# Optimization experiments

Hardware: AMD Instinct MI355X
Metric: run time of the kernel (lower is better)

The kernel has to match this reference:

```python
import jax, jax.numpy as jnp
import numpy as np
from jax import lax

B, F_BINS, T = 4, 128, 16384
J_T, N_W, KF, KT = 4, 8, 33, 129


def setup_inputs() -> dict:
    key = jax.random.key(0)
    k1, k2, k3 = jax.random.split(key, 3)
    x = jax.random.normal(k1, (B, F_BINS, T), dtype=jnp.float32)
    # complex Morlet-style wavelet bank parameters: [J_t, n_w, kf, kt]
    wav_real = jax.random.normal(k2, (J_T, N_W, KF, KT), dtype=jnp.float32) * 0.05
    wav_imag = jax.random.normal(k3, (J_T, N_W, KF, KT), dtype=jnp.float32) * 0.05
    return {"x": x, "wav_real": wav_real, "wav_imag": wav_imag}


def _avg_pool_last(x, w):
    # non-overlapping mean pooling along the last (time) axis, stride == window
    if w == 1:
        return x
    shp = x.shape
    return x.reshape(shp[:-1] + (shp[-1] // w, w)).mean(axis=-1)


def reference(x, wav_real, wav_imag):
    # x: [B, F, T]; wav_real/wav_imag: [J_t, n_w, kf, kt]
    J_t, n_w = wav_real.shape[0], wav_real.shape[1]
    # avg_win_t cascade: 2**J_t halving each octave -> [16, 8, 4, 2]
    avg_wins_t = [2 ** (J_t - j) for j in range(J_t)]
    xi = x[:, None]  # [B, 1, F, T_cur]
    octaves = []
    for j in range(J_t):
        # stack real and imag kernels as 2*n_w output channels of one conv2d
        k = jnp.concatenate([wav_real[j], wav_imag[j]], axis=0)[:, None]  # [2*n_w, 1, kf, kt]
        o = lax.conv_general_dilated(
            xi, k, window_strides=(1, 1), padding='SAME',
            dimension_numbers=('NCHW', 'OIHW', 'NCHW'))  # [B, 2*n_w, F, T_cur]
        # complex modulus (x is real, kernel complex): |conv_r + i*conv_i|
        mod = jnp.sqrt(o[:, :n_w] ** 2 + o[:, n_w:] ** 2)  # [B, n_w, F, T_cur]
        w = avg_wins_t[j]
        octaves.append(_avg_pool_last(mod, w))  # [B, n_w, F, T//2**J_t]
        if w > 1:
            xi = _avg_pool_last(xi, 2)  # decimate input in time by 2
    # all octaves share the same pooled time length -> concat on channel dim
    return jnp.concatenate(octaves, axis=1)  # [B, J_t*n_w, F, T//2**J_t]
```

## Files before the change

kernel.cpp:

```cpp
#include <hip/hip_runtime.h>
#include <math.h>

#define B_      4
#define F_BINS  128
#define T_FULL  16384
#define NW      8
#define KF      33
#define KT      129

#define TT      128
#define ROWS    260
#define PITCH   72
#define DTP     136
#define D2      48

typedef __attribute__((ext_vector_type(8))) short short8;
typedef __attribute__((ext_vector_type(4))) float f32x4;
typedef uint uint4a16 __attribute__((ext_vector_type(4), aligned(16)));

union ABFrag { uint4a16 u; short8 v; };

__device__ __forceinline__ ushort f2bf(float v) {
  unsigned u = __float_as_uint(v);
  unsigned r = (u + 0x7FFFu + ((u >> 16) & 1u)) >> 16;
  return (ushort)r;
}

__device__ __forceinline__ short8 load_a16(const ushort* p) {
  ABFrag f; f.u = *(const uint4a16*)p; return f.v;
}

__device__ __forceinline__ short8 mkG(short8 a, short8 b) {
  return __builtin_shufflevector(a, b, 4, 5, 6, 7, 8, 9, 10, 11);
}

__global__ __launch_bounds__(256) void prep_w(
    const float* __restrict__ wr, const float* __restrict__ wi,
    ushort* __restrict__ wq) {
  int idx = blockIdx.x * 256 + threadIdx.x;
  int d2  = idx % D2;
  int dt  = (idx / D2) % DTP;
  int ch  = (idx / (D2 * DTP)) % 16;
  int gam = (idx / (D2 * DTP * 16)) % 4;
  int oct = idx / (D2 * DTP * 16 * 4);
  int df  = d2 - 4 - gam;
  float v = 0.f;
  if (df >= 0 && df < KF && dt < KT) {
    const float* src = (ch < 8) ? wr : wi;
    v = src[(((size_t)oct * 8 + (ch & 7)) * KF + df) * KT + dt];
  }
  wq[idx] = f2bf(v);
}

__global__ __launch_bounds__(256) void prep_x(
    const float* __restrict__ x,
    ushort* __restrict__ xT0, ushort* __restrict__ xT1,
    ushort* __restrict__ xT2, ushort* __restrict__ xT3) {
  __shared__ float lt[128 * 65];
  const int b  = blockIdx.y;
  const int t0 = blockIdx.x * 64;
  const int tid = threadIdx.x;
  const int wv = tid >> 6, lane = tid & 63;
#pragma unroll
  for (int rep = 0; rep < 32; ++rep) {
    int f = rep * 4 + wv;
    lt[f * 65 + lane] = x[((size_t)b * 128 + f) * T_FULL + t0 + lane];
  }
  __syncthreads();
  ushort* dst[4] = {xT0, xT1, xT2, xT3};
  const int Ts[4] = {16384, 8192, 4096, 2048};
  for (int lvl = 0; lvl < 4; ++lvl) {
    int nt = 64 >> lvl, w = 1 << lvl;
    float inv = 1.f / (float)w;
    int tasks = nt * 16;
    for (int i = tid; i < tasks; i += 256) {
      int tl = i >> 4, fc = i & 15;
      __align__(16) ushort vs[8];
#pragma unroll
      for (int e = 0; e < 8; ++e) {
        float a = 0.f;
        for (int m = 0; m < w; ++m) a += lt[(fc * 8 + e) * 65 + tl * w + m];
        vs[e] = f2bf(a * inv);
      }
      ushort* pdst = dst[lvl] + ((size_t)b * Ts[lvl] + (t0 >> lvl) + tl) * 128 + fc * 8;
      *(uint4*)pdst = *(const uint4*)vs;
    }
  }
}

__global__ __launch_bounds__(256, 3) void conv_mfma(
    const ushort* __restrict__ xT0, const ushort* __restrict__ xT1,
    const ushort* __restrict__ xT2, const ushort* __restrict__ xT3,
    const ushort* __restrict__ wq, float* __restrict__ out) {
  __shared__ ushort xt[ROWS * PITCH];
  const int tid = threadIdx.x;
  const int bx = blockIdx.x;

  int oct, local;
  if (bx < 2048)      { oct = 0; local = bx; }
  else if (bx < 3072) { oct = 1; local = bx - 2048; }
  else if (bx < 3584) { oct = 2; local = bx - 3072; }
  else                { oct = 3; local = bx - 3584; }
  const ushort* xT = (oct == 0) ? xT0 : (oct == 1) ? xT1 : (oct == 2) ? xT2 : xT3;
  const int Tj = T_FULL >> oct;
  const int lw = 4 - oct;
  const int nxs = 7 - oct;
  const int tx = local & ((1 << nxs) - 1);
  const int rest = local >> nxs;
  const int t0 = tx * TT;
  const int f0 = (rest & 3) * 32;
  const int b  = rest >> 2;

  for (int i = tid; i < ROWS * 8; i += 256) {
    int row = i >> 3, fc = i & 7;
    int t = t0 - 64 + row;
    int f = f0 - 16 + fc * 8;
    uint4 v = make_uint4(0u, 0u, 0u, 0u);
    if (t >= 0 && t < Tj && f >= 0 && f < 128)
      v = *(const uint4*)(xT + ((size_t)b * Tj + t) * 128 + f);
    *(uint4*)&xt[row * PITCH + fc * 8] = v;
  }
  __syncthreads();

  const int wave = tid >> 6, lane = tid & 63;
  const int p = lane & 15;
  const int g = lane >> 4;
  const int hi = (lane >= 32);
  const float invw = 1.0f / (float)(1 << lw);

  for (int gamma = 0; gamma < 4; ++gamma) {
    const ushort* wbase = wq + ((((size_t)oct * 4 + gamma) * 16 + p) * DTP + g) * D2;
    const ushort* wp = wbase + 4 * D2;
    int rb = (p + g) * PITCH + wave * (32 * PITCH);

    f32x4 acc[8][2];
#pragma unroll
    for (int k = 0; k < 8; ++k)
#pragma unroll
      for (int r = 0; r < 2; ++r) { f32x4 z = {0.f, 0.f, 0.f, 0.f}; acc[k][r] = z; }

    short8 F[6], G[5];
#pragma unroll
    for (int u = 0; u < 6; ++u) F[u] = load_a16(wbase + 8 * u);
    G[0] = mkG(F[0], F[1]);
    G[1] = mkG(F[1], F[2]);

#pragma unroll 1
    for (int c = 0; c < 33; ++c) {
      __builtin_amdgcn_s_setprio(1);
      const int SLO[8] = {0, 0, 1, 1, 2, 2, 3, 3};
#pragma unroll
      for (int s = 0; s < 8; ++s) {
        if (s == 0) G[2] = mkG(F[2], F[3]);
        if (s == 1) G[3] = mkG(F[3], F[4]);
        if (s == 2) G[4] = mkG(F[4], F[5]);
        short8 bv0 = *(const short8*)&xt[rb + s * 8];
        short8 bv1 = *(const short8*)&xt[rb + 16 * PITCH + s * 8];
#pragma unroll
        for (int k = 0; k < 8; ++k) {
          if (s >= SLO[k] && s <= SLO[k] + 4) {
            const int idx = s - SLO[k];
            short8 a = (k & 1) ? F[idx] : G[idx];
            acc[k][0] = __builtin_amdgcn_mfma_f32_16x16x32_bf16(a, bv0, acc[k][0], 0, 0, 0);
            acc[k][1] = __builtin_amdgcn_mfma_f32_16x16x32_bf16(a, bv1, acc[k][1], 0, 0, 0);
          }
        }
        if (s >= 3) F[s - 3] = load_a16(wp + 8 * (s - 3));
        if (s == 6) G[0] = mkG(F[0], F[1]);
        if (s == 7) G[1] = mkG(F[1], F[2]);
      }
      F[5] = load_a16(wp + 40);
      __builtin_amdgcn_s_setprio(0);
      wp += 4 * D2;
      rb += 4 * PITCH;
    }

#pragma unroll
    for (int k = 0; k < 8; ++k) {
      const int fo = f0 + gamma + 4 * k;
#pragma unroll
      for (int fr = 0; fr < 2; ++fr) {
        const int tbase = t0 + 32 * wave + 16 * fr;
        float sq[4];
#pragma unroll
        for (int r = 0; r < 4; ++r) {
          float a = acc[k][fr][r];
          float o = __shfl_xor(a, 32);
          sq[r] = a * a + o * o;
        }
        float m0 = sqrtf(hi ? sq[2] : sq[0]);
        float m1 = sqrtf(hi ? sq[3] : sq[1]);
        if (lw == 4) { m0 += __shfl_xor(m0, 8); m1 += __shfl_xor(m1, 8); }
        if (lw >= 3) { m0 += __shfl_xor(m0, 4); m1 += __shfl_xor(m1, 4); }
        if (lw >= 2) { m0 += __shfl_xor(m0, 2); m1 += __shfl_xor(m1, 2); }
        m0 += __shfl_xor(m0, 1);  m1 += __shfl_xor(m1, 1);
        if ((p & ((1 << lw) - 1)) == 0) {
          const int ch0 = 4 * (g & 1) + (hi ? 2 : 0);
          const int tcol = (tbase + p) >> lw;
          size_t o0 = (((size_t)b * 32 + oct * 8 + ch0) * 128 + fo) * 1024 + tcol;
          out[o0] = m0 * invw;
          out[o0 + (size_t)128 * 1024] = m1 * invw;
        }
      }
    }
  }
}

extern "C" void kernel_launch(void* const* d_in, const int* in_sizes, int n_in,
                              void* d_out, int out_size, void* d_ws, size_t ws_size,
                              hipStream_t stream) {
  const float* x  = (const float*)d_in[0];
  const float* wr = (const float*)d_in[1];
  const float* wi = (const float*)d_in[2];
  float* out = (float*)d_out;

  ushort* xT0 = (ushort*)d_ws;
  ushort* xT1 = xT0 + (size_t)4 * 16384 * 128;
  ushort* xT2 = xT1 + (size_t)4 * 8192 * 128;
  ushort* xT3 = xT2 + (size_t)4 * 4096 * 128;
  ushort* wq  = xT3 + (size_t)4 * 2048 * 128;

  prep_w<<<1671168 / 256, 256, 0, stream>>>(wr, wi, wq);
  prep_x<<<dim3(T_FULL / 64, B_), 256, 0, stream>>>(x, xT0, xT1, xT2, xT3);

  conv_mfma<<<3840, 256, 0, stream>>>(xT0, xT1, xT2, xT3, wq, out);
}
```

Before: 1.599 ms.

## Switch conv inner loop to 32x32x16 MFMA with reorganized weight layout

Replaces the 16x16x32 bf16 MFMA tiling with 32x32x16 MFMA tiles, restructuring the weight pre-layout (gamma/phase split, smaller DTP padding) and the loop order (2 gammas x 2 frequency halves, 65 time steps of 2). The larger MFMA shape is meant to raise operand reuse per instruction and cut LDS reads and A-fragment shuffles per FLOP. The epilogue is rewritten to pair real/imag from within one accumulator and pool along the lane dimension. Risks include higher register pressure from 64-float accumulators and a more serialized MFMA dependency chain.

Result: slower. 2.675 ms (+67.3%).

```diff
diff --git a/kernel.cpp b/kernel.cpp
--- a/kernel.cpp
+++ b/kernel.cpp
@@ -4,18 +4,17 @@
 #define B_      4
 #define F_BINS  128
 #define T_FULL  16384
-#define NW      8
 #define KF      33
 #define KT      129
 
 #define TT      128
 #define ROWS    260
 #define PITCH   72
-#define DTP     136
+#define DTP     132
 #define D2      48
 
-typedef __attribute__((ext_vector_type(8))) short short8;
-typedef __attribute__((ext_vector_type(4))) float f32x4;
+typedef __attribute__((ext_vector_type(8)))  short short8;
+typedef __attribute__((ext_vector_type(16))) float f32x16;
 typedef uint uint4a16 __attribute__((ext_vector_type(4), aligned(16)));
 
 union ABFrag { uint4a16 u; short8 v; };
@@ -41,9 +40,10 @@
   int d2  = idx % D2;
   int dt  = (idx / D2) % DTP;
   int ch  = (idx / (D2 * DTP)) % 16;
-  int gam = (idx / (D2 * DTP * 16)) % 4;
-  int oct = idx / (D2 * DTP * 16 * 4);
-  int df  = d2 - 4 - gam;
+  int ps  = (idx / (D2 * DTP * 16)) % 2;
+  int gam = (idx / (D2 * DTP * 16 * 2)) % 2;
+  int oct = idx / (D2 * DTP * 16 * 2 * 2);
+  int df  = d2 - 4 - gam - 2 * ps;
   float v = 0.f;
   if (df >= 0 && df < KF && dt < KT) {
     const float* src = (ch < 8) ? wr : wi;
@@ -102,10 +102,10 @@
   else if (bx < 3584) { oct = 2; local = bx - 3072; }
   else                { oct = 3; local = bx - 3584; }
   const ushort* xT = (oct == 0) ? xT0 : (oct == 1) ? xT1 : (oct == 2) ? xT2 : xT3;
-  const int Tj = T_FULL >> oct;
-  const int lw = 4 - oct;
+  const int Tj  = T_FULL >> oct;
+  const int lw  = 4 - oct;
   const int nxs = 7 - oct;
-  const int tx = local & ((1 << nxs) - 1);
+  const int tx   = local & ((1 << nxs) - 1);
   const int rest = local >> nxs;
   const int t0 = tx * TT;
   const int f0 = (rest & 3) * 32;
@@ -123,83 +123,76 @@
   __syncthreads();
 
   const int wave = tid >> 6, lane = tid & 63;
-  const int p = lane & 15;
-  const int g = lane >> 4;
-  const int hi = (lane >= 32);
+  const int n  = lane & 31;
+  const int h  = lane >> 5;
+  const int ch = lane & 15;
+  const int ps = (lane >> 4) & 1;
   const float invw = 1.0f / (float)(1 << lw);
 
-  for (int gamma = 0; gamma < 4; ++gamma) {
-    const ushort* wbase = wq + ((((size_t)oct * 4 + gamma) * 16 + p) * DTP + g) * D2;
-    const ushort* wp = wbase + 4 * D2;
-    int rb = (p + g) * PITCH + wave * (32 * PITCH);
-
-    f32x4 acc[8][2];
-#pragma unroll
-    for (int k = 0; k < 8; ++k)
-#pragma unroll
-      for (int r = 0; r < 2; ++r) { f32x4 z = {0.f, 0.f, 0.f, 0.f}; acc[k][r] = z; }
-
-    short8 F[6], G[5];
-#pragma unroll
-    for (int u = 0; u < 6; ++u) F[u] = load_a16(wbase + 8 * u);
-    G[0] = mkG(F[0], F[1]);
-    G[1] = mkG(F[1], F[2]);
+  for (int gam = 0; gam < 2; ++gam) {
+    for (int kh = 0; kh < 2; ++kh) {
+      const ushort* wp =
+          wq + ((((size_t)((oct * 2 + gam) * 2 + ps)) * 16 + ch) * DTP + h) * D2;
+      int rb = (32 * wave + n + h) * PITCH + 16 * kh;
+
+      f32x16 acc[4];
+#pragma unroll
+      for (int q = 0; q < 4; ++q)
+#pragma unroll
+        for (int e = 0; e < 16; ++e) acc[q][e] = 0.f;
+
+      short8 F[6];
+#pragma unroll
+      for (int u = 0; u < 6; ++u) F[u] = load_a16(wp + 8 * u);
+      wp += 2 * D2;
 
 #pragma unroll 1
-    for (int c = 0; c < 33; ++c) {
-      __builtin_amdgcn_s_setprio(1);
-      const int SLO[8] = {0, 0, 1, 1, 2, 2, 3, 3};
-#pragma unroll
-      for (int s = 0; s < 8; ++s) {
-        if (s == 0) G[2] = mkG(F[2], F[3]);
-        if (s == 1) G[3] = mkG(F[3], F[4]);
-        if (s == 2) G[4] = mkG(F[4], F[5]);
-        short8 bv0 = *(const short8*)&xt[rb + s * 8];
-        short8 bv1 = *(const short8*)&xt[rb + 16 * PITCH + s * 8];
-#pragma unroll
-        for (int k = 0; k < 8; ++k) {
-          if (s >= SLO[k] && s <= SLO[k] + 4) {
-            const int idx = s - SLO[k];
-            short8 a = (k & 1) ? F[idx] : G[idx];
-            acc[k][0] = __builtin_amdgcn_mfma_f32_16x16x32_bf16(a, bv0, acc[k][0], 0, 0, 0);
-            acc[k][1] = __builtin_amdgcn_mfma_f32_16x16x32_bf16(a, bv1, acc[k][1], 0, 0, 0);
+      for (int c = 0; c < 65; ++c) {
+        short8 G[5];
+#pragma unroll
+        for (int u = 0; u < 5; ++u) G[u] = mkG(F[u], F[u + 1]);
+        __builtin_amdgcn_s_setprio(1);
+#pragma unroll
+        for (int s = 0; s < 6; ++s) {
+          short8 bv = *(const short8*)&xt[rb + s * 8];
+          if (s <= 4) {
+            acc[0] = __builtin_amdgcn_mfma_f32_32x32x16_bf16(G[s], bv, acc[0], 0, 0, 0);
+            acc[1] = __builtin_amdgcn_mfma_f32_32x32x16_bf16(F[s], bv, acc[1], 0, 0, 0);
           }
+          if (s >= 1) {
+            acc[2] = __builtin_amdgcn_mfma_f32_32x32x16_bf16(G[s - 1], bv, acc[2], 0, 0, 0);
+            acc[3] = __builtin_amdgcn_mfma_f32_32x32x16_bf16(F[s - 1], bv, acc[3], 0, 0, 0);
+          }
+          if (s >= 2) F[s - 2] = load_a16(wp + 8 * (s - 2));
         }
-        if (s >= 3) F[s - 3] = load_a16(wp + 8 * (s - 3));
-        if (s == 6) G[0] = mkG(F[0], F[1]);
-        if (s == 7) G[1] = mkG(F[1], F[2]);
+        F[4] = load_a16(wp + 32);
+        F[5] = load_a16(wp + 40);
+        __builtin_amdgcn_s_setprio(0);
+        wp += 2 * D2;
+        rb += 2 * PITCH;
       }
-      F[5] = load_a16(wp + 40);
-      __builtin_amdgcn_s_setprio(0);
-      wp += 4 * D2;
-      rb += 4 * PITCH;
-    }
-
-#pragma unroll
-    for (int k = 0; k < 8; ++k) {
-      const int fo = f0 + gamma + 4 * k;
-#pragma unroll
-      for (int fr = 0; fr < 2; ++fr) {
-        const int tbase = t0 + 32 * wave + 16 * fr;
-        float sq[4];
-#pragma unroll
-        for (int r = 0; r < 4; ++r) {
-          float a = acc[k][fr][r];
-          float o = __shfl_xor(a, 32);
-          sq[r] = a * a + o * o;
-        }
-        float m0 = sqrtf(hi ? sq[2] : sq[0]);
-        float m1 = sqrtf(hi ? sq[3] : sq[1]);
-        if (lw == 4) { m0 += __shfl_xor(m0, 8); m1 += __shfl_xor(m1, 8); }
-        if (lw >= 3) { m0 += __shfl_xor(m0, 4); m1 += __shfl_xor(m1, 4); }
-        if (lw >= 2) { m0 += __shfl_xor(m0, 2); m1 += __shfl_xor(m1, 2); }
-        m0 += __shfl_xor(m0, 1);  m1 += __shfl_xor(m1, 1);
-        if ((p & ((1 << lw) - 1)) == 0) {
-          const int ch0 = 4 * (g & 1) + (hi ? 2 : 0);
-          const int tcol = (tbase + p) >> lw;
-          size_t o0 = (((size_t)b * 32 + oct * 8 + ch0) * 128 + fo) * 1024 + tcol;
-          out[o0] = m0 * invw;
-          out[o0 + (size_t)128 * 1024] = m1 * invw;
+
+#pragma unroll
+      for (int q = 0; q < 4; ++q) {
+#pragma unroll
+        for (int p2 = 0; p2 < 2; ++p2) {
+          const int fo = f0 + gam + 16 * kh + 4 * q + 2 * p2;
+#pragma unroll
+          for (int bi = 0; bi < 4; ++bi) {
+            float re = acc[q][8 * p2 + bi];
+            float im = acc[q][8 * p2 + 4 + bi];
+            float m = sqrtf(re * re + im * im);
+            m += __shfl_xor(m, 1);
+            if (lw >= 2) m += __shfl_xor(m, 2);
+            if (lw >= 3) m += __shfl_xor(m, 4);
+            if (lw >= 4) m += __shfl_xor(m, 8);
+            if ((n & ((1 << lw) - 1)) == 0) {
+              const int wvl = 4 * h + bi;
+              const int tcol = (t0 + 32 * wave + n) >> lw;
+              out[(((size_t)b * 32 + oct * 8 + wvl) * 128 + fo) * 1024 + tcol] =
+                  m * invw;
+            }
+          }
         }
       }
     }
@@ -220,7 +213,7 @@
   ushort* xT3 = xT2 + (size_t)4 * 4096 * 128;
   ushort* wq  = xT3 + (size_t)4 * 2048 * 128;
 
-  prep_w<<<1671168 / 256, 256, 0, stream>>>(wr, wi, wq);
+  prep_w<<<1622016 / 256, 256, 0, stream>>>(wr, wi, wq);
   prep_x<<<dim3(T_FULL / 64, B_), 256, 0, stream>>>(x, xT0, xT1, xT2, xT3);
 
   conv_mfma<<<3840, 256, 0, stream>>>(xT0, xT1, xT2, xT3, wq, out);
```

## Halve time tile and process two gamma phases per pass sharing B fragments

Applied to the files above, without the earlier changes.

Shrinks the time tile from 128 to 64, doubling the grid. Each wave now covers 16 time rows and processes two gamma phases at once, so one LDS B fragment feeds two weight sets instead of one weight set feeding two time fragments. The fifth G fragment is now loaded directly from a repacked weight layout (prep_w shifts entries at d2>=40) instead of being built by a shuffle. This trades LDS reads against weight register and global traffic and makes the smaller tiles load more halo overhead.

After: 2.720 ms. +70.2%, slower.

```diff
diff --git a/kernel.cpp b/kernel.cpp
--- a/kernel.cpp
+++ b/kernel.cpp
@@ -4,15 +4,14 @@
 #define B_      4
 #define F_BINS  128
 #define T_FULL  16384
-#define NW      8
 #define KF      33
 #define KT      129
 
-#define TT      128
-#define ROWS    260
+#define TT      64
+#define ROWS    196
 #define PITCH   72
 #define DTP     136
-#define D2      48
+#define D2R     48
 
 typedef __attribute__((ext_vector_type(8))) short short8;
 typedef __attribute__((ext_vector_type(4))) float f32x4;
@@ -38,12 +37,12 @@
     const float* __restrict__ wr, const float* __restrict__ wi,
     ushort* __restrict__ wq) {
   int idx = blockIdx.x * 256 + threadIdx.x;
-  int d2  = idx % D2;
-  int dt  = (idx / D2) % DTP;
-  int ch  = (idx / (D2 * DTP)) % 16;
-  int gam = (idx / (D2 * DTP * 16)) % 4;
-  int oct = idx / (D2 * DTP * 16 * 4);
-  int df  = d2 - 4 - gam;
+  int d2  = idx % D2R;
+  int dt  = (idx / D2R) % DTP;
+  int ch  = (idx / (D2R * DTP)) % 16;
+  int gam = (idx / (D2R * DTP * 16)) % 4;
+  int oct = idx / (D2R * DTP * 16 * 4);
+  int df  = d2 - 4 - gam - (d2 >= 40 ? 4 : 0);
   float v = 0.f;
   if (df >= 0 && df < KF && dt < KT) {
     const float* src = (ch < 8) ? wr : wi;
@@ -96,16 +95,15 @@
   const int tid = threadIdx.x;
   const int bx = blockIdx.x;
 
-  int oct, local;
-  if (bx < 2048)      { oct = 0; local = bx; }
-  else if (bx < 3072) { oct = 1; local = bx - 2048; }
-  else if (bx < 3584) { oct = 2; local = bx - 3072; }
-  else                { oct = 3; local = bx - 3584; }
+  int oct, local, nxs;
+  if (bx < 4096)      { oct = 0; local = bx;        nxs = 8; }
+  else if (bx < 6144) { oct = 1; local = bx - 4096; nxs = 7; }
+  else if (bx < 7168) { oct = 2; local = bx - 6144; nxs = 6; }
+  else                { oct = 3; local = bx - 7168; nxs = 5; }
   const ushort* xT = (oct == 0) ? xT0 : (oct == 1) ? xT1 : (oct == 2) ? xT2 : xT3;
-  const int Tj = T_FULL >> oct;
-  const int lw = 4 - oct;
-  const int nxs = 7 - oct;
-  const int tx = local & ((1 << nxs) - 1);
+  const int Tj  = T_FULL >> oct;
+  const int lw  = 4 - oct;
+  const int tx   = local & ((1 << nxs) - 1);
   const int rest = local >> nxs;
   const int t0 = tx * TT;
   const int f0 = (rest & 3) * 32;
@@ -128,22 +126,34 @@
   const int hi = (lane >= 32);
   const float invw = 1.0f / (float)(1 << lw);
 
-  for (int gamma = 0; gamma < 4; ++gamma) {
-    const ushort* wbase = wq + ((((size_t)oct * 4 + gamma) * 16 + p) * DTP + g) * D2;
-    const ushort* wp = wbase + 4 * D2;
-    int rb = (p + g) * PITCH + wave * (32 * PITCH);
-
-    f32x4 acc[8][2];
-#pragma unroll
-    for (int k = 0; k < 8; ++k)
-#pragma unroll
-      for (int r = 0; r < 2; ++r) { f32x4 z = {0.f, 0.f, 0.f, 0.f}; acc[k][r] = z; }
-
-    short8 F[6], G[5];
-#pragma unroll
-    for (int u = 0; u < 6; ++u) F[u] = load_a16(wbase + 8 * u);
-    G[0] = mkG(F[0], F[1]);
-    G[1] = mkG(F[1], F[2]);
+  for (int gp = 0; gp < 2; ++gp) {
+    const int gA = 2 * gp, gB = 2 * gp + 1;
+    const ushort* wpA = wq + ((((size_t)oct * 4 + gA) * 16 + p) * DTP + g) * D2R;
+    const ushort* wpB = wq + ((((size_t)oct * 4 + gB) * 16 + p) * DTP + g) * D2R;
+    int rb = (p + g) * PITCH + wave * (16 * PITCH);
+
+    f32x4 aA[8], aB[8];
+#pragma unroll
+    for (int k = 0; k < 8; ++k) {
+      f32x4 z = {0.f, 0.f, 0.f, 0.f};
+      aA[k] = z; aB[k] = z;
+    }
+
+    short8 FA[5], GA[5], FB[5], GB[5];
+#pragma unroll
+    for (int u = 0; u < 5; ++u) {
+      FA[u] = load_a16(wpA + 8 * u);
+      FB[u] = load_a16(wpB + 8 * u);
+    }
+    GA[4] = load_a16(wpA + 40);
+    GB[4] = load_a16(wpB + 40);
+#pragma unroll
+    for (int u = 0; u < 4; ++u) {
+      GA[u] = mkG(FA[u], FA[u + 1]);
+      GB[u] = mkG(FB[u], FB[u + 1]);
+    }
+    wpA += 4 * D2R;
+    wpB += 4 * D2R;
 
 #pragma unroll 1
     for (int c = 0; c < 33; ++c) {
@@ -151,40 +161,44 @@
       const int SLO[8] = {0, 0, 1, 1, 2, 2, 3, 3};
 #pragma unroll
       for (int s = 0; s < 8; ++s) {
-        if (s == 0) G[2] = mkG(F[2], F[3]);
-        if (s == 1) G[3] = mkG(F[3], F[4]);
-        if (s == 2) G[4] = mkG(F[4], F[5]);
-        short8 bv0 = *(const short8*)&xt[rb + s * 8];
-        short8 bv1 = *(const short8*)&xt[rb + 16 * PITCH + s * 8];
+        short8 bv = *(const short8*)&xt[rb + s * 8];
 #pragma unroll
         for (int k = 0; k < 8; ++k) {
           if (s >= SLO[k] && s <= SLO[k] + 4) {
             const int idx = s - SLO[k];
-            short8 a = (k & 1) ? F[idx] : G[idx];
-            acc[k][0] = __builtin_amdgcn_mfma_f32_16x16x32_bf16(a, bv0, acc[k][0], 0, 0, 0);
-            acc[k][1] = __builtin_amdgcn_mfma_f32_16x16x32_bf16(a, bv1, acc[k][1], 0, 0, 0);
+            aA[k] = __builtin_amdgcn_mfma_f32_16x16x32_bf16(
+                (k & 1) ? FA[idx] : GA[idx], bv, aA[k], 0, 0, 0);
+            aB[k] = __builtin_amdgcn_mfma_f32_16x16x32_bf16(
+                (k & 1) ? FB[idx] : GB[idx], bv, aB[k], 0, 0, 0);
           }
         }
-        if (s >= 3) F[s - 3] = load_a16(wp + 8 * (s - 3));
-        if (s == 6) G[0] = mkG(F[0], F[1]);
-        if (s == 7) G[1] = mkG(F[1], F[2]);
+        if (s == 0) { GA[2] = mkG(FA[2], FA[3]); GB[2] = mkG(FB[2], FB[3]); }
+        if (s == 1) { GA[3] = mkG(FA[3], FA[4]); GB[3] = mkG(FB[3], FB[4]); }
+        if (s >= 3) {
+          FA[s - 3] = load_a16(wpA + 8 * (s - 3));
+          FB[s - 3] = load_a16(wpB + 8 * (s - 3));
+        }
+        if (s == 6) { GA[0] = mkG(FA[0], FA[1]); GB[0] = mkG(FB[0], FB[1]); }
+        if (s == 7) {
+          GA[1] = mkG(FA[1], FA[2]); GB[1] = mkG(FB[1], FB[2]);
+          GA[4] = load_a16(wpA + 40); GB[4] = load_a16(wpB + 40);
+        }
       }
-      F[5] = load_a16(wp + 40);
       __builtin_amdgcn_s_setprio(0);
-      wp += 4 * D2;
-      rb += 4 * PITCH;
-    }
-
-#pragma unroll
-    for (int k = 0; k < 8; ++k) {
-      const int fo = f0 + gamma + 4 * k;
-#pragma unroll
-      for (int fr = 0; fr < 2; ++fr) {
-        const int tbase = t0 + 32 * wave + 16 * fr;
+      wpA += 4 * D2R;
+      wpB += 4 * D2R;
+      rb  += 4 * PITCH;
+    }
+
+    auto epi = [&](f32x4 (&acc)[8], int gamma) {
+#pragma unroll
+      for (int k = 0; k < 8; ++k) {
+        const int fo = f0 + gamma + 4 * k;
+        const int tbase = t0 + 16 * wave;
         float sq[4];
 #pragma unroll
         for (int r = 0; r < 4; ++r) {
-          float a = acc[k][fr][r];
+          float a = acc[k][r];
           float o = __shfl_xor(a, 32);
           sq[r] = a * a + o * o;
         }
@@ -202,7 +216,9 @@
           out[o0 + (size_t)128 * 1024] = m1 * invw;
         }
       }
-    }
+    };
+    epi(aA, gA);
+    epi(aB, gB);
   }
 }
 
@@ -223,5 +239,5 @@
   prep_w<<<1671168 / 256, 256, 0, stream>>>(wr, wi, wq);
   prep_x<<<dim3(T_FULL / 64, B_), 256, 0, stream>>>(x, xT0, xT1, xT2, xT3);
 
-  conv_mfma<<<3840, 256, 0, stream>>>(xT0, xT1, xT2, xT3, wq, out);
-}
+  conv_mfma<<<7680, 256, 0, stream>>>(xT0, xT1, xT2, xT3, wq, out);
+}
```
